# Kernel tuning notes

Hardware: AMD Instinct MI355X
Metric: run time of the kernel (lower is better)

Reference implementation:

```python
import jax, jax.numpy as jnp
import numpy as np

DIM = 512
HIDDEN = 1024
NUM_EXPERTS = 8
TOP_K = 2
BALANCE_LOSS_WEIGHT = 0.01


def setup_inputs() -> dict:
    key = jax.random.key(0)
    ks = jax.random.split(key, 6)
    B, S = 4, 8192
    x = jax.random.normal(ks[0], (B, S, DIM), dtype=jnp.float32)
    # Linear params (stored already transposed for x @ W convenience)
    scale_in = 1.0 / np.sqrt(DIM)
    scale_hid = 1.0 / np.sqrt(HIDDEN)
    gate_w = jax.random.uniform(ks[1], (DIM, NUM_EXPERTS), jnp.float32, -scale_in, scale_in)
    w1 = jax.random.uniform(ks[2], (NUM_EXPERTS, DIM, HIDDEN), jnp.float32, -scale_in, scale_in)
    b1 = jax.random.uniform(ks[3], (NUM_EXPERTS, HIDDEN), jnp.float32, -scale_in, scale_in)
    w2 = jax.random.uniform(ks[4], (NUM_EXPERTS, HIDDEN, DIM), jnp.float32, -scale_hid, scale_hid)
    b2 = jax.random.uniform(ks[5], (NUM_EXPERTS, DIM), jnp.float32, -scale_hid, scale_hid)
    return {"x": x, "gate_w": gate_w, "w1": w1, "b1": b1, "w2": w2, "b2": b2}


def reference(x, gate_w, w1, b1, w2, b2):
    B, S, D = x.shape
    T = B * S
    E = gate_w.shape[1]
    flat_x = x.reshape(T, D)

    # Gating (eval mode: no noise)
    gate_logits = flat_x @ gate_w                      # [T, E]
    gates = jax.nn.softmax(gate_logits, axis=-1)
    top_k_gates, top_k_indices = jax.lax.top_k(gates, TOP_K)
    top_k_gates = top_k_gates / jnp.sum(top_k_gates, axis=-1, keepdims=True)

    rows = jnp.arange(T)[:, None]
    # Per-token combine weight for each expert (0 if not selected)
    combine_w = jnp.zeros((T, E), flat_x.dtype).at[rows, top_k_indices].add(top_k_gates)
    # Load-balance loss (indices are discrete -> constant mask)
    expert_mask = jnp.zeros((T, E), flat_x.dtype).at[rows, top_k_indices].set(1.0)
    expert_usage = expert_mask.sum(0) / T
    balance_loss = jnp.mean((expert_usage - 1.0 / E) ** 2) * E * BALANCE_LOSS_WEIGHT

    # Expert MLPs; unselected tokens have combine weight 0 so contribute nothing,
    # matching the original masked gather/scatter math exactly.
    out = jnp.zeros_like(flat_x)
    for e in range(E):  # small fixed expert count
        h = jax.nn.gelu(flat_x @ w1[e] + b1[e], approximate=False)  # [T, HIDDEN]
        out = out + (h @ w2[e] + b2[e]) * combine_w[:, e:e + 1]
    return out.reshape(B, S, D), balance_loss
```

## Files before the change

### kernel.cpp

```cpp
#include <hip/hip_runtime.h>
#include <stdint.h>

#define T_TOK 32768
#define DDIM 512
#define HID 1024
#define NEXP 8
#define BKT 32

typedef _Float16 f16;
typedef _Float16 f16x8 __attribute__((ext_vector_type(8)));
typedef _Float16 f16x4 __attribute__((ext_vector_type(4)));
typedef float f32x4 __attribute__((ext_vector_type(4)));

__device__ __forceinline__ void gload_lds16(const void* g, void* l) {
  __builtin_amdgcn_global_load_lds(
      (__attribute__((address_space(1))) void*)g,
      (__attribute__((address_space(3))) void*)l, 16, 0, 0);
}

__global__ void k_cvt_x(const float* __restrict__ x, f16* __restrict__ xh) {
  int i = blockIdx.x * blockDim.x + threadIdx.x;
  float4 v = ((const float4*)x)[i];
  f16x4 o = {(f16)v.x, (f16)v.y, (f16)v.z, (f16)v.w};
  ((f16x4*)xh)[i] = o;
}

__global__ void k_transpose(const float* __restrict__ W, f16* __restrict__ Wt,
                            const int K, const int N) {
  __shared__ float tile[64][65];
  const int e = blockIdx.z;
  const float* Wb = W + (size_t)e * K * N;
  f16* Wtb = Wt + (size_t)e * K * N;
  const int k0 = blockIdx.x * 64, n0 = blockIdx.y * 64;
  const int tr = threadIdx.x >> 2;
  const int tc = (threadIdx.x & 3) * 16;
#pragma unroll
  for (int j = 0; j < 16; j += 4) {
    float4 v = *(const float4*)&Wb[(size_t)(k0 + tr) * N + n0 + tc + j];
    tile[tr][tc + j + 0] = v.x; tile[tr][tc + j + 1] = v.y;
    tile[tr][tc + j + 2] = v.z; tile[tr][tc + j + 3] = v.w;
  }
  __syncthreads();
  f16x8 t0, t1;
#pragma unroll
  for (int j = 0; j < 8; ++j) {
    t0[j] = (f16)tile[tc + j][tr];
    t1[j] = (f16)tile[tc + 8 + j][tr];
  }
  *(f16x8*)&Wtb[(size_t)(n0 + tr) * K + k0 + tc] = t0;
  *(f16x8*)&Wtb[(size_t)(n0 + tr) * K + k0 + tc + 8] = t1;
}

__global__ void k_gate(const float* __restrict__ x, const float* __restrict__ gw,
                       int* __restrict__ route_e, float* __restrict__ route_w,
                       int* __restrict__ cnt) {
  __shared__ int scnt[NEXP];
  const int tid = threadIdx.x, lane = tid & 63, wv = tid >> 6;
  if (tid < NEXP) scnt[tid] = 0;
  __syncthreads();

  float ga[4][8], gb[4][8];
#pragma unroll
  for (int j = 0; j < 4; ++j) {
    const int r0 = lane * 4 + j;
    const int r1 = 256 + lane * 4 + j;
    float4 q0 = *(const float4*)&gw[r0 * 8];
    float4 q1 = *(const float4*)&gw[r0 * 8 + 4];
    ga[j][0] = q0.x; ga[j][1] = q0.y; ga[j][2] = q0.z; ga[j][3] = q0.w;
    ga[j][4] = q1.x; ga[j][5] = q1.y; ga[j][6] = q1.z; ga[j][7] = q1.w;
    q0 = *(const float4*)&gw[r1 * 8];
    q1 = *(const float4*)&gw[r1 * 8 + 4];
    gb[j][0] = q0.x; gb[j][1] = q0.y; gb[j][2] = q0.z; gb[j][3] = q0.w;
    gb[j][4] = q1.x; gb[j][5] = q1.y; gb[j][6] = q1.z; gb[j][7] = q1.w;
  }

  const int tbase = blockIdx.x * 32 + wv * 8;
  for (int it = 0; it < 8; ++it) {
    const int t = tbase + it;
    const float4 A = *(const float4*)&x[(size_t)t * DDIM + lane * 4];
    const float4 B = *(const float4*)&x[(size_t)t * DDIM + 256 + lane * 4];
    float p[8];
#pragma unroll
    for (int e = 0; e < 8; ++e) {
      p[e] = A.x * ga[0][e] + A.y * ga[1][e] + A.z * ga[2][e] + A.w * ga[3][e] +
             B.x * gb[0][e] + B.y * gb[1][e] + B.z * gb[2][e] + B.w * gb[3][e];
    }
#pragma unroll
    for (int off = 32; off >= 1; off >>= 1) {
#pragma unroll
      for (int e = 0; e < 8; ++e) p[e] += __shfl_xor(p[e], off);
    }
    if (lane == 0) {
      int e1 = 0;
#pragma unroll
      for (int e = 1; e < 8; ++e) if (p[e] > p[e1]) e1 = e;
      int e2 = (e1 == 0) ? 1 : 0;
#pragma unroll
      for (int e = 0; e < 8; ++e) if (e != e1 && p[e] > p[e2]) e2 = e;
      const float wa = 1.0f / (1.0f + expf(p[e2] - p[e1]));
      route_e[t] = e1 | (e2 << 8);
      route_w[t] = wa;
      atomicAdd(&scnt[e1], 1);
      atomicAdd(&scnt[e2], 1);
    }
  }
  __syncthreads();
  if (tid < NEXP) atomicAdd(&cnt[tid], scnt[tid]);
}

__global__ void k_scan(const int* __restrict__ cnt, int* __restrict__ base,
                       int* __restrict__ cursor, float* __restrict__ out_loss) {
  if (threadIdx.x == 0) {
    int b = 0;
    float loss = 0.0f;
    for (int e = 0; e < NEXP; ++e) {
      base[e] = b;
      cursor[e] = b;
      b += cnt[e];
      float u = (float)cnt[e] / (float)T_TOK - 0.125f;
      loss += u * u;
    }
    *out_loss = loss * 0.01f;
  }
}

__global__ void k_scatter(const int* __restrict__ route_e, const float* __restrict__ route_w,
                          int* __restrict__ cursor, int* __restrict__ tok_slot,
                          float* __restrict__ wgt_slot) {
  const int t = blockIdx.x * blockDim.x + threadIdx.x;
  const int lane = threadIdx.x & 63;
  const int re = route_e[t];
  const float wa = route_w[t];
  const int e1 = re & 0xff, e2 = re >> 8;
#pragma unroll
  for (int e = 0; e < NEXP; ++e) {
    unsigned long long m = __ballot(e1 == e);
    if (m) {
      const int leader = __ffsll(m) - 1;
      int b0 = 0;
      if (lane == leader) b0 = atomicAdd(&cursor[e], __popcll(m));
      b0 = __shfl(b0, leader);
      if (e1 == e) {
        const int pos = b0 + __popcll(m & ((1ull << lane) - 1));
        tok_slot[pos] = t;
        wgt_slot[pos] = wa;
      }
    }
    m = __ballot(e2 == e);
    if (m) {
      const int leader = __ffsll(m) - 1;
      int b0 = 0;
      if (lane == leader) b0 = atomicAdd(&cursor[e], __popcll(m));
      b0 = __shfl(b0, leader);
      if (e2 == e) {
        const int pos = b0 + __popcll(m & ((1ull << lane) - 1));
        tok_slot[pos] = t;
        wgt_slot[pos] = 1.0f - wa;
      }
    }
  }
}


#define STAGE_T(t_)                                                  \
  do {                                                               \
    f16* _ldsA = &lds[((t_) & 3) * 16384];                           \
    f16* _ldsB = _ldsA + 8192;                                       \
    const int _k = (t_) * BKT;                                       \
    gload_lds16(aSrc[0] + _k, _ldsA + (wv * 2 + 0) * 512);           \
    gload_lds16(aSrc[1] + _k, _ldsA + (wv * 2 + 1) * 512);           \
    gload_lds16(bSrc[0] + _k, _ldsB + (wv * 2 + 0) * 512);           \
    gload_lds16(bSrc[1] + _k, _ldsB + (wv * 2 + 1) * 512);           \
  } while (0)

#define COMPUTE_T(t_)                                                             \
  do {                                                                            \
    const f16* _A = &lds[((t_) & 3) * 16384];                                     \
    const f16* _B = _A + 8192;                                                    \
    f16x8 af[8], bf[4];                                                           \
    _Pragma("unroll") for (int mf = 0; mf < 8; ++mf) {                            \
      const int row = wm * 128 + mf * 16 + l15;                                   \
      af[mf] = *(const f16x8*)&_A[row * 32 + ((g ^ (row & 3)) * 8)];              \
    }                                                                             \
    _Pragma("unroll") for (int nf = 0; nf < 4; ++nf) {                            \
      const int row = wn * 64 + nf * 16 + l15;                                    \
      bf[nf] = *(const f16x8*)&_B[row * 32 + ((g ^ (row & 3)) * 8)];              \
    }                                                                             \
    _Pragma("unroll") for (int mf = 0; mf < 8; ++mf)                              \
      _Pragma("unroll") for (int nf = 0; nf < 4; ++nf)                            \
        acc[mf][nf] =                                                             \
            __builtin_amdgcn_mfma_f32_16x16x32_f16(af[mf], bf[nf], acc[mf][nf], 0, 0, 0); \
  } while (0)

#define PIPE_LOOP(NT_)                                               \
  do {                                                               \
    STAGE_T(0); STAGE_T(1); STAGE_T(2);                              \
    for (int t = 0; t < (NT_); ++t) {                                \
      const int rem = (NT_)-1 - t;                                   \
      if (rem >= 2)                                                  \
        asm volatile("s_waitcnt vmcnt(8)" ::: "memory");             \
      else if (rem == 1)                                             \
        asm volatile("s_waitcnt vmcnt(4)" ::: "memory");             \
      else                                                           \
        asm volatile("s_waitcnt vmcnt(0)" ::: "memory");             \
      __builtin_amdgcn_s_barrier();                                  \
      __builtin_amdgcn_sched_barrier(0);                             \
      COMPUTE_T(t);                                                  \
      if (t + 3 < (NT_)) STAGE_T(t + 3);                             \
    }                                                                \
  } while (0)

__global__ __launch_bounds__(512, 2) void k_mlp1(
    const f16* __restrict__ xh, const f16* __restrict__ w1t,
    const float* __restrict__ b1, f16* __restrict__ h,
    const int* __restrict__ tok_slot, const int* __restrict__ base,
    const int* __restrict__ cnt, const int hc, const int c0) {
  const int lid = blockIdx.x;
  const int e = lid & 7;
  const int q = lid >> 3;
  const int mt = q & 63;
  const int nt = q >> 6;
  const int ne = cnt[e];
  const int n0 = nt * 256;
  const int sbase = base[e];
  const int shi = sbase + ne;

  __shared__ f16 lds[4 * 16384];

  const int tid = threadIdx.x;
  const int lane = tid & 63;
  const int wv = tid >> 6;
  const int wm = wv >> 2, wn = wv & 3;
  const int g = lane >> 4;
  const int l15 = lane & 15;
  const int lr = lane >> 2;
  const int lc = lane & 3;

  for (int m0 = mt * 256; m0 < ne; m0 += 64 * 256) {
    const int slot0 = sbase + m0;

    const f16* aSrc[2];
    const f16* bSrc[2];
#pragma unroll
    for (int i = 0; i < 2; ++i) {
      const int row = (wv * 2 + i) * 16 + lr;
      const int ch = lc ^ (row & 3);
      int slot = slot0 + row;
      slot = (slot <= shi - 1) ? slot : (shi - 1);
      const int tok = tok_slot[slot];
      aSrc[i] = xh + (size_t)tok * DDIM + ch * 8;
      bSrc[i] = w1t + (size_t)(e * HID + c0 + n0 + row) * DDIM + ch * 8;
    }

    f32x4 acc[8][4];
#pragma unroll
    for (int a = 0; a < 8; ++a)
#pragma unroll
      for (int b = 0; b < 4; ++b) { f32x4 z = {0.f, 0.f, 0.f, 0.f}; acc[a][b] = z; }

    PIPE_LOOP(DDIM / BKT);

#pragma unroll
    for (int mf = 0; mf < 8; ++mf) {
#pragma unroll
      for (int r = 0; r < 4; ++r) {
        const int row = wm * 128 + mf * 16 + g * 4 + r;
        const int slot = slot0 + row;
        if (slot >= shi) continue;
#pragma unroll
        for (int nf = 0; nf < 4; ++nf) {
          const int col = wn * 64 + nf * 16 + l15;
          float v = acc[mf][nf][r] + b1[e * HID + c0 + n0 + col];
          v = 0.5f * v * (1.0f + erff(v * 0.70710678118654752f));
          h[(size_t)slot * hc + n0 + col] = (f16)v;
        }
      }
    }
  }
}

__global__ __launch_bounds__(512, 2) void k_mlp2(
    const f16* __restrict__ h, const f16* __restrict__ w2t,
    const float* __restrict__ b2, float* __restrict__ out,
    const int* __restrict__ tok_slot, const float* __restrict__ wgt_slot,
    const int* __restrict__ base, const int* __restrict__ cnt,
    const int hc, const int c0) {
  const int lid = blockIdx.x;
  const int e = lid & 7;
  const int q = lid >> 3;
  const int mt = q & 63;
  const int nt = q >> 6;
  const int ne = cnt[e];
  const int n0 = nt * 256;
  const int sbase = base[e];
  const int shi = sbase + ne;

  __shared__ f16 lds[4 * 16384];

  const int tid = threadIdx.x;
  const int lane = tid & 63;
  const int wv = tid >> 6;
  const int wm = wv >> 2, wn = wv & 3;
  const int g = lane >> 4;
  const int l15 = lane & 15;
  const int lr = lane >> 2;
  const int lc = lane & 3;

  for (int m0 = mt * 256; m0 < ne; m0 += 64 * 256) {
    const int slot0 = sbase + m0;

    const f16* aSrc[2];
    const f16* bSrc[2];
#pragma unroll
    for (int i = 0; i < 2; ++i) {
      const int row = (wv * 2 + i) * 16 + lr;
      const int ch = lc ^ (row & 3);
      int slot = slot0 + row;
      slot = (slot <= 2 * T_TOK - 1) ? slot : (2 * T_TOK - 1);
      aSrc[i] = h + (size_t)slot * hc + ch * 8;
      bSrc[i] = w2t + (size_t)(e * DDIM + n0 + row) * HID + c0 + ch * 8;
    }

    f32x4 acc[8][4];
#pragma unroll
    for (int a = 0; a < 8; ++a)
#pragma unroll
      for (int b = 0; b < 4; ++b) { f32x4 z = {0.f, 0.f, 0.f, 0.f}; acc[a][b] = z; }

    PIPE_LOOP(hc / BKT);

#pragma unroll
    for (int mf = 0; mf < 8; ++mf) {
#pragma unroll
      for (int r = 0; r < 4; ++r) {
        const int row = wm * 128 + mf * 16 + g * 4 + r;
        const int slot = slot0 + row;
        if (slot >= shi) continue;
        const int tok = tok_slot[slot];
        const float w = wgt_slot[slot];
        float* orow = out + (size_t)tok * DDIM + n0;
#pragma unroll
        for (int nf = 0; nf < 4; ++nf) {
          const int col = wn * 64 + nf * 16 + l15;
          float v = acc[mf][nf][r];
          if (c0 == 0) v += b2[e * DDIM + n0 + col];
          unsafeAtomicAdd(orow + col, w * v);
        }
      }
    }
  }
}

extern "C" void kernel_launch(void* const* d_in, const int* in_sizes, int n_in,
                              void* d_out, int out_size, void* d_ws, size_t ws_size,
                              hipStream_t stream) {
  (void)in_sizes; (void)n_in;
  const float* x  = (const float*)d_in[0];
  const float* gw = (const float*)d_in[1];
  const float* w1 = (const float*)d_in[2];
  const float* b1 = (const float*)d_in[3];
  const float* w2 = (const float*)d_in[4];
  const float* b2 = (const float*)d_in[5];
  float* out = (float*)d_out;

  char* ws = (char*)d_ws;
  size_t off = 0;
  auto alloc = [&](size_t bytes) {
    char* p = ws + off;
    off += (bytes + 255) & ~(size_t)255;
    return p;
  };
  f16*   xh       = (f16*)  alloc((size_t)T_TOK * DDIM * 2);
  f16*   w1t      = (f16*)  alloc((size_t)NEXP * DDIM * HID * 2);
  f16*   w2t      = (f16*)  alloc((size_t)NEXP * DDIM * HID * 2);
  int*   route_e  = (int*)  alloc((size_t)T_TOK * 4);
  float* route_w  = (float*)alloc((size_t)T_TOK * 4);
  int*   tok_slot = (int*)  alloc((size_t)2 * T_TOK * 4);
  float* wgt_slot = (float*)alloc((size_t)2 * T_TOK * 4);
  int*   cnt      = (int*)  alloc(256);
  int*   base     = cnt + 8;
  int*   cursor   = cnt + 16;
  f16*   hbuf     = (f16*)(ws + off);
  const size_t havail = (ws_size > off) ? (ws_size - off) : 0;

  int ns = 4;
  const int cands[3] = {1, 2, 4};
  for (int i = 0; i < 3; ++i) {
    if ((size_t)2 * T_TOK * (HID / cands[i]) * 2 <= havail) { ns = cands[i]; break; }
  }
  const int hc = HID / ns;

  hipMemsetAsync(cnt, 0, 32, stream);
  hipMemsetAsync(d_out, 0, (size_t)out_size * sizeof(float), stream);

  k_cvt_x<<<dim3(T_TOK * DDIM / 4 / 256), 256, 0, stream>>>(x, xh);
  k_transpose<<<dim3(DDIM / 64, HID / 64, NEXP), 256, 0, stream>>>(w1, w1t, DDIM, HID);
  k_transpose<<<dim3(HID / 64, DDIM / 64, NEXP), 256, 0, stream>>>(w2, w2t, HID, DDIM);
  k_gate<<<dim3(T_TOK / 32), 256, 0, stream>>>(x, gw, route_e, route_w, cnt);
  k_scan<<<1, 64, 0, stream>>>(cnt, base, cursor, out + (size_t)T_TOK * DDIM);
  k_scatter<<<dim3(T_TOK / 256), 256, 0, stream>>>(route_e, route_w, cursor, tok_slot, wgt_slot);

  for (int c = 0; c < ns; ++c) {
    k_mlp1<<<dim3(8 * 64 * (hc / 256)), 512, 0, stream>>>(
        xh, w1t, b1, hbuf, tok_slot, base, cnt, hc, c * hc);
    k_mlp2<<<dim3(8 * 64 * 2), 512, 0, stream>>>(
        hbuf, w2t, b2, out, tok_slot, wgt_slot, base, cnt, hc, c * hc);
  }
}
```

Before: 673.6 us.

## Split K-loop into half-tile phases interleaving LDS reads, staging and MFMA clusters

Replaces the per-tile stage/compute pipeline with a finer schedule. Each 32-wide K chunk is processed in two halves of the M fragments, with the next chunk's A and B global-to-LDS loads issued between the MFMA clusters, and the MFMA clusters run at raised wave priority. A and B get separate LDS arrays, and the LDS swizzle changes to use (row>>1)&3. The grid halves the m-tile count, so blocks loop over larger expert segments. The aim is better overlap of memory traffic, LDS reads and matrix math, in exchange for more barriers and fewer blocks in flight when expert segments are short.

```diff
diff --git a/kernel.cpp b/kernel.cpp
--- a/kernel.cpp
+++ b/kernel.cpp
@@ -5,7 +5,6 @@
 #define DDIM 512
 #define HID 1024
 #define NEXP 8
-#define BKT 32
 
 typedef _Float16 f16;
 typedef _Float16 f16x8 __attribute__((ext_vector_type(8)));
@@ -162,52 +161,72 @@
 }
 
 
-#define STAGE_T(t_)                                                  \
-  do {                                                               \
-    f16* _ldsA = &lds[((t_) & 3) * 16384];                           \
-    f16* _ldsB = _ldsA + 8192;                                       \
-    const int _k = (t_) * BKT;                                       \
-    gload_lds16(aSrc[0] + _k, _ldsA + (wv * 2 + 0) * 512);           \
-    gload_lds16(aSrc[1] + _k, _ldsA + (wv * 2 + 1) * 512);           \
-    gload_lds16(bSrc[0] + _k, _ldsB + (wv * 2 + 0) * 512);           \
-    gload_lds16(bSrc[1] + _k, _ldsB + (wv * 2 + 1) * 512);           \
-  } while (0)
-
-#define COMPUTE_T(t_)                                                             \
-  do {                                                                            \
-    const f16* _A = &lds[((t_) & 3) * 16384];                                     \
-    const f16* _B = _A + 8192;                                                    \
-    f16x8 af[8], bf[4];                                                           \
-    _Pragma("unroll") for (int mf = 0; mf < 8; ++mf) {                            \
-      const int row = wm * 128 + mf * 16 + l15;                                   \
-      af[mf] = *(const f16x8*)&_A[row * 32 + ((g ^ (row & 3)) * 8)];              \
-    }                                                                             \
-    _Pragma("unroll") for (int nf = 0; nf < 4; ++nf) {                            \
-      const int row = wn * 64 + nf * 16 + l15;                                    \
-      bf[nf] = *(const f16x8*)&_B[row * 32 + ((g ^ (row & 3)) * 8)];              \
-    }                                                                             \
-    _Pragma("unroll") for (int mf = 0; mf < 8; ++mf)                              \
-      _Pragma("unroll") for (int nf = 0; nf < 4; ++nf)                            \
-        acc[mf][nf] =                                                             \
-            __builtin_amdgcn_mfma_f32_16x16x32_f16(af[mf], bf[nf], acc[mf][nf], 0, 0, 0); \
-  } while (0)
-
-#define PIPE_LOOP(NT_)                                               \
-  do {                                                               \
-    STAGE_T(0); STAGE_T(1); STAGE_T(2);                              \
-    for (int t = 0; t < (NT_); ++t) {                                \
-      const int rem = (NT_)-1 - t;                                   \
-      if (rem >= 2)                                                  \
-        asm volatile("s_waitcnt vmcnt(8)" ::: "memory");             \
-      else if (rem == 1)                                             \
-        asm volatile("s_waitcnt vmcnt(4)" ::: "memory");             \
-      else                                                           \
-        asm volatile("s_waitcnt vmcnt(0)" ::: "memory");             \
-      __builtin_amdgcn_s_barrier();                                  \
-      __builtin_amdgcn_sched_barrier(0);                             \
-      COMPUTE_T(t);                                                  \
-      if (t + 3 < (NT_)) STAGE_T(t + 3);                             \
-    }                                                                \
+#define VM8 asm volatile("s_waitcnt vmcnt(8)" ::: "memory")
+#define VM4 asm volatile("s_waitcnt vmcnt(4)" ::: "memory")
+#define VM0 asm volatile("s_waitcnt vmcnt(0)" ::: "memory")
+#define BARR __builtin_amdgcn_s_barrier()
+
+#define STAGE_A(h_) do { const int _sl = (h_) & 3;                          \
+    gload_lds16(aP0 + (h_) * 32, &AS[_sl * 8192 + (wv * 2 + 0) * 512]);     \
+    gload_lds16(aP1 + (h_) * 32, &AS[_sl * 8192 + (wv * 2 + 1) * 512]); } while (0)
+#define STAGE_B(h_) do { const int _sl = (h_) & 3;                          \
+    gload_lds16(bP0 + (h_) * 32, &BS[_sl * 8192 + (wv * 2 + 0) * 512]);     \
+    gload_lds16(bP1 + (h_) * 32, &BS[_sl * 8192 + (wv * 2 + 1) * 512]); } while (0)
+
+#define RD_AF(mfh_, h_) do { const int _sl = (h_) & 3;                      \
+    _Pragma("unroll") for (int mf = 0; mf < 4; ++mf) {                      \
+      const int row = wm * 128 + (mfh_) * 64 + mf * 16 + l15;               \
+      af[mf] = *(const f16x8*)&AS[_sl * 8192 + row * 32 + ((g ^ ((row >> 1) & 3)) * 8)]; \
+    } } while (0)
+#define RD_BF(h_) do { const int _sl = (h_) & 3;                            \
+    _Pragma("unroll") for (int nf = 0; nf < 4; ++nf) {                      \
+      const int row = wn * 64 + nf * 16 + l15;                              \
+      bf[nf] = *(const f16x8*)&BS[_sl * 8192 + row * 32 + ((g ^ ((row >> 1) & 3)) * 8)]; \
+    } } while (0)
+
+#define CLUSTER(mfh_) do {                                                  \
+    __builtin_amdgcn_s_setprio(1);                                          \
+    _Pragma("unroll") for (int mf = 0; mf < 4; ++mf)                        \
+      _Pragma("unroll") for (int nf = 0; nf < 4; ++nf)                      \
+        acc[(mfh_) * 4 + mf][nf] = __builtin_amdgcn_mfma_f32_16x16x32_f16(  \
+            af[mf], bf[nf], acc[(mfh_) * 4 + mf][nf], 0, 0, 0);             \
+    __builtin_amdgcn_s_setprio(0); } while (0)
+
+#define K_LOOP(NT_) do {                                                    \
+    BARR;                      \
+    STAGE_A(0); STAGE_B(0); STAGE_A(1); STAGE_B(1); STAGE_A(2); STAGE_B(2); \
+    for (int T = 0; T < (NT_) - 1; ++T) {                                   \
+      const int h0 = 2 * T, h1 = 2 * T + 1;                                 \
+      VM8; BARR;                                                            \
+      RD_AF(0, h0); RD_BF(h0);                                              \
+      STAGE_A(h1 + 2);                                                      \
+      CLUSTER(0);                                                           \
+      BARR;                                                                 \
+      RD_AF(1, h0);                                                         \
+      STAGE_B(h1 + 2);                                                      \
+      CLUSTER(1);                                                           \
+      VM8; BARR;                                                            \
+      RD_AF(0, h1); RD_BF(h1);                                              \
+      if (T < (NT_) - 2) STAGE_A(h1 + 3);                                   \
+      CLUSTER(0);                                                           \
+      BARR;                                                                 \
+      RD_AF(1, h1);                                                         \
+      if (T < (NT_) - 2) STAGE_B(h1 + 3);                                   \
+      CLUSTER(1);                                                           \
+    }                                                                       \
+    { const int h0 = 2 * (NT_) - 2, h1 = 2 * (NT_) - 1;                     \
+      VM4; BARR;                                                            \
+      RD_AF(0, h0); RD_BF(h0);                                              \
+      CLUSTER(0);                                                           \
+      BARR;                                                                 \
+      RD_AF(1, h0);                                                         \
+      CLUSTER(1);                                                           \
+      VM0; BARR;                                                            \
+      RD_AF(0, h1); RD_BF(h1);                                              \
+      CLUSTER(0);                                                           \
+      BARR;                                                                 \
+      RD_AF(1, h1);                                                         \
+      CLUSTER(1); }                                                         \
   } while (0)
 
 __global__ __launch_bounds__(512, 2) void k_mlp1(
@@ -215,17 +234,17 @@
     const float* __restrict__ b1, f16* __restrict__ h,
     const int* __restrict__ tok_slot, const int* __restrict__ base,
     const int* __restrict__ cnt, const int hc, const int c0) {
-  const int lid = blockIdx.x;
-  const int e = lid & 7;
-  const int q = lid >> 3;
-  const int mt = q & 63;
-  const int nt = q >> 6;
+  const int e = blockIdx.x & 7;
+  const int q = blockIdx.x >> 3;
+  const int mt = q & 31;
+  const int nt = q >> 5;
   const int ne = cnt[e];
   const int n0 = nt * 256;
   const int sbase = base[e];
   const int shi = sbase + ne;
 
-  __shared__ f16 lds[4 * 16384];
+  __shared__ f16 AS[4 * 8192];
+  __shared__ f16 BS[4 * 8192];
 
   const int tid = threadIdx.x;
   const int lane = tid & 63;
@@ -233,46 +252,44 @@
   const int wm = wv >> 2, wn = wv & 3;
   const int g = lane >> 4;
   const int l15 = lane & 15;
-  const int lr = lane >> 2;
-  const int lc = lane & 3;
-
-  for (int m0 = mt * 256; m0 < ne; m0 += 64 * 256) {
+
+  const int sr0 = (wv * 2 + 0) * 16 + (lane >> 2);
+  const int sr1 = (wv * 2 + 1) * 16 + (lane >> 2);
+  const int sc0 = (lane & 3) ^ ((sr0 >> 1) & 3);
+  const int sc1 = (lane & 3) ^ ((sr1 >> 1) & 3);
+
+  const f16* bP0 = w1t + (size_t)(e * HID + c0 + n0 + sr0) * DDIM + sc0 * 8;
+  const f16* bP1 = w1t + (size_t)(e * HID + c0 + n0 + sr1) * DDIM + sc1 * 8;
+
+  for (int m0 = mt * 256; m0 < ne; m0 += 8192) {
     const int slot0 = sbase + m0;
-
-    const f16* aSrc[2];
-    const f16* bSrc[2];
-#pragma unroll
-    for (int i = 0; i < 2; ++i) {
-      const int row = (wv * 2 + i) * 16 + lr;
-      const int ch = lc ^ (row & 3);
-      int slot = slot0 + row;
-      slot = (slot <= shi - 1) ? slot : (shi - 1);
-      const int tok = tok_slot[slot];
-      aSrc[i] = xh + (size_t)tok * DDIM + ch * 8;
-      bSrc[i] = w1t + (size_t)(e * HID + c0 + n0 + row) * DDIM + ch * 8;
-    }
+    int s0 = slot0 + sr0; s0 = (s0 <= shi - 1) ? s0 : (shi - 1);
+    int s1 = slot0 + sr1; s1 = (s1 <= shi - 1) ? s1 : (shi - 1);
+    const f16* aP0 = xh + (size_t)tok_slot[s0] * DDIM + sc0 * 8;
+    const f16* aP1 = xh + (size_t)tok_slot[s1] * DDIM + sc1 * 8;
 
     f32x4 acc[8][4];
 #pragma unroll
     for (int a = 0; a < 8; ++a)
 #pragma unroll
       for (int b = 0; b < 4; ++b) { f32x4 z = {0.f, 0.f, 0.f, 0.f}; acc[a][b] = z; }
-
-    PIPE_LOOP(DDIM / BKT);
+    f16x8 af[4], bf[4];
+
+    K_LOOP(DDIM / 64);
 
 #pragma unroll
     for (int mf = 0; mf < 8; ++mf) {
 #pragma unroll
       for (int r = 0; r < 4; ++r) {
         const int row = wm * 128 + mf * 16 + g * 4 + r;
-        const int slot = slot0 + row;
-        if (slot >= shi) continue;
+        const int oslot = slot0 + row;
+        if (oslot >= shi) continue;
 #pragma unroll
         for (int nf = 0; nf < 4; ++nf) {
           const int col = wn * 64 + nf * 16 + l15;
           float v = acc[mf][nf][r] + b1[e * HID + c0 + n0 + col];
           v = 0.5f * v * (1.0f + erff(v * 0.70710678118654752f));
-          h[(size_t)slot * hc + n0 + col] = (f16)v;
+          h[(size_t)oslot * hc + n0 + col] = (f16)v;
         }
       }
     }
@@ -285,17 +302,17 @@
     const int* __restrict__ tok_slot, const float* __restrict__ wgt_slot,
     const int* __restrict__ base, const int* __restrict__ cnt,
     const int hc, const int c0) {
-  const int lid = blockIdx.x;
-  const int e = lid & 7;
-  const int q = lid >> 3;
-  const int mt = q & 63;
-  const int nt = q >> 6;
+  const int e = blockIdx.x & 7;
+  const int q = blockIdx.x >> 3;
+  const int mt = q & 31;
+  const int nt = q >> 5;
   const int ne = cnt[e];
   const int n0 = nt * 256;
   const int sbase = base[e];
   const int shi = sbase + ne;
 
-  __shared__ f16 lds[4 * 16384];
+  __shared__ f16 AS[4 * 8192];
+  __shared__ f16 BS[4 * 8192];
 
   const int tid = threadIdx.x;
   const int lane = tid & 63;
@@ -303,41 +320,40 @@
   const int wm = wv >> 2, wn = wv & 3;
   const int g = lane >> 4;
   const int l15 = lane & 15;
-  const int lr = lane >> 2;
-  const int lc = lane & 3;
-
-  for (int m0 = mt * 256; m0 < ne; m0 += 64 * 256) {
+
+  const int sr0 = (wv * 2 + 0) * 16 + (lane >> 2);
+  const int sr1 = (wv * 2 + 1) * 16 + (lane >> 2);
+  const int sc0 = (lane & 3) ^ ((sr0 >> 1) & 3);
+  const int sc1 = (lane & 3) ^ ((sr1 >> 1) & 3);
+
+  const f16* bP0 = w2t + (size_t)(e * DDIM + n0 + sr0) * HID + c0 + sc0 * 8;
+  const f16* bP1 = w2t + (size_t)(e * DDIM + n0 + sr1) * HID + c0 + sc1 * 8;
+
+  for (int m0 = mt * 256; m0 < ne; m0 += 8192) {
     const int slot0 = sbase + m0;
-
-    const f16* aSrc[2];
-    const f16* bSrc[2];
-#pragma unroll
-    for (int i = 0; i < 2; ++i) {
-      const int row = (wv * 2 + i) * 16 + lr;
-      const int ch = lc ^ (row & 3);
-      int slot = slot0 + row;
-      slot = (slot <= 2 * T_TOK - 1) ? slot : (2 * T_TOK - 1);
-      aSrc[i] = h + (size_t)slot * hc + ch * 8;
-      bSrc[i] = w2t + (size_t)(e * DDIM + n0 + row) * HID + c0 + ch * 8;
-    }
+    int s0 = slot0 + sr0; s0 = (s0 <= shi - 1) ? s0 : (shi - 1);
+    int s1 = slot0 + sr1; s1 = (s1 <= shi - 1) ? s1 : (shi - 1);
+    const f16* aP0 = h + (size_t)s0 * hc + sc0 * 8;
+    const f16* aP1 = h + (size_t)s1 * hc + sc1 * 8;
 
     f32x4 acc[8][4];
 #pragma unroll
     for (int a = 0; a < 8; ++a)
 #pragma unroll
       for (int b = 0; b < 4; ++b) { f32x4 z = {0.f, 0.f, 0.f, 0.f}; acc[a][b] = z; }
-
-    PIPE_LOOP(hc / BKT);
+    f16x8 af[4], bf[4];
+
+    K_LOOP(hc / 64);
 
 #pragma unroll
     for (int mf = 0; mf < 8; ++mf) {
 #pragma unroll
       for (int r = 0; r < 4; ++r) {
         const int row = wm * 128 + mf * 16 + g * 4 + r;
-        const int slot = slot0 + row;
-        if (slot >= shi) continue;
-        const int tok = tok_slot[slot];
-        const float w = wgt_slot[slot];
+        const int oslot = slot0 + row;
+        if (oslot >= shi) continue;
+        const int tok = tok_slot[oslot];
+        const float w = wgt_slot[oslot];
         float* orow = out + (size_t)tok * DDIM + n0;
 #pragma unroll
         for (int nf = 0; nf < 4; ++nf) {
@@ -401,9 +417,9 @@
   k_scatter<<<dim3(T_TOK / 256), 256, 0, stream>>>(route_e, route_w, cursor, tok_slot, wgt_slot);
 
   for (int c = 0; c < ns; ++c) {
-    k_mlp1<<<dim3(8 * 64 * (hc / 256)), 512, 0, stream>>>(
+    k_mlp1<<<dim3(8 * 32 * (hc / 256)), 512, 0, stream>>>(
         xh, w1t, b1, hbuf, tok_slot, base, cnt, hc, c * hc);
-    k_mlp2<<<dim3(8 * 64 * 2), 512, 0, stream>>>(
+    k_mlp2<<<dim3(8 * 32 * (DDIM / 256)), 512, 0, stream>>>(
         hbuf, w2t, b2, out, tok_slot, wgt_slot, base, cnt, hc, c * hc);
   }
 }
```

After: 722.2 us. +7.2%, slower.
